# Optimization experiments

Hardware: AMD Instinct MI355X
Metric: run time of the kernel (lower is better)

## Reference

```python
import jax, jax.numpy as jnp
import numpy as np

BN_EPS = 1e-5

def _conv1x1(x, w, b):
    # x: [B,C,H,W], w: [O,C], b: [O]
    return jnp.einsum('bchw,oc->bohw', x, w) + b[None, :, None, None]

def _maxpool2x2(x):
    B, C, H, W = x.shape
    return x.reshape(B, C, H // 2, 2, W // 2, 2).max(axis=(3, 5))

def setup_inputs() -> dict:
    key = jax.random.key(0)
    ks = jax.random.split(key, 6)
    B, C, H, W = 8, 256, 64, 64
    Ci = C // 2  # inter_channels default
    x = jax.random.normal(ks[0], (B, C, H, W), jnp.float32)
    s = lambda k, sh: jax.random.normal(k, sh, jnp.float32) * 0.02
    return {
        'x': x,
        'w_g': s(ks[1], (Ci, C)), 'b_g': jnp.zeros((Ci,), jnp.float32),
        'w_theta': s(ks[2], (Ci, C)), 'b_theta': jnp.zeros((Ci,), jnp.float32),
        'w_phi': s(ks[3], (Ci, C)), 'b_phi': jnp.zeros((Ci,), jnp.float32),
        'w_w': s(ks[4], (C, Ci)), 'b_w': jnp.zeros((C,), jnp.float32),
        'bn_gamma': 1.0 + 0.1 * jax.random.normal(ks[5], (C,), jnp.float32),
        'bn_beta': jnp.zeros((C,), jnp.float32),
    }

def reference(x, w_g, b_g, w_theta, b_theta, w_phi, b_phi, w_w, b_w, bn_gamma, bn_beta):
    B, C, H, W = x.shape
    Ci = w_g.shape[0]
    # projections (sub_sample=True: maxpool 2x2 on g and phi)
    g_x = _maxpool2x2(_conv1x1(x, w_g, b_g)).reshape(B, Ci, -1)          # [B,Ci,M]
    g_x = g_x.transpose(0, 2, 1)                                          # [B,M,Ci]
    theta_x = _conv1x1(x, w_theta, b_theta).reshape(B, Ci, -1)            # [B,Ci,N]
    theta_x = theta_x.transpose(0, 2, 1)                                  # [B,N,Ci]
    phi_x = _maxpool2x2(_conv1x1(x, w_phi, b_phi)).reshape(B, Ci, -1)     # [B,Ci,M]
    # unscaled embedded-Gaussian attention (no 1/sqrt(d), as in source)
    f = jnp.einsum('bnc,bcm->bnm', theta_x, phi_x)                        # [B,N,M]
    f_div_C = jax.nn.softmax(f, axis=-1)
    y = jnp.einsum('bnm,bmc->bnc', f_div_C, g_x)                          # [B,N,Ci]
    y = y.transpose(0, 2, 1).reshape(B, Ci, H, W)
    # W: 1x1 conv + BatchNorm (training mode: batch statistics)
    wy = _conv1x1(y, w_w, b_w)                                            # [B,C,H,W]
    mean = wy.mean(axis=(0, 2, 3), keepdims=True)
    var = wy.var(axis=(0, 2, 3), keepdims=True)
    wy = (wy - mean) * jax.lax.rsqrt(var + BN_EPS)
    wy = wy * bn_gamma[None, :, None, None] + bn_beta[None, :, None, None]
    return wy + x
```

## Files before the change

### kernel.cpp

```cpp
#include <hip/hip_runtime.h>
#include <hip/hip_bf16.h>

#define NB 8
#define NC 256
#define NCI 128
#define NSP 4096
#define NM 1024

typedef float f32x4 __attribute__((ext_vector_type(4)));
typedef float f32x16 __attribute__((ext_vector_type(16)));
typedef short s16x8 __attribute__((ext_vector_type(8)));
typedef unsigned short u16;

#define OFF_XH  (0ull)
#define OFF_THT (33554432ull)
#define OFF_PHT (41943040ull)
#define OFF_GP  (44040192ull)
#define OFF_YH  (46137344ull)
#define OFF_YL  (54525952ull)
#define OFF_WY  (0ull)
#define OFF_WBH (62914560ull)
#define OFF_WBL (63111168ull)
#define OFF_WWH (63307776ull)
#define OFF_WWL (63373312ull)
#define OFF_S   (63438848ull)

#define GLL(src, dst) __builtin_amdgcn_global_load_lds( \
    (const __attribute__((address_space(1))) unsigned*)(src), \
    (__attribute__((address_space(3))) unsigned*)(dst), 16, 0, 0)

__device__ __forceinline__ u16 f2bf(float f) {
  union { __hip_bfloat16 h; u16 u; } v;
  v.h = __float2bfloat16(f);
  return v.u;
}
__device__ __forceinline__ float bf2f(u16 u) {
  union { unsigned u; float f; } v;
  v.u = (unsigned)u << 16;
  return v.f;
}
__device__ __forceinline__ u16 bfmax4(u16 a, u16 b, u16 c, u16 d) {
  float v = fmaxf(fmaxf(bf2f(a), bf2f(b)), fmaxf(bf2f(c), bf2f(d)));
  return f2bf(v);
}
__device__ __forceinline__ unsigned cvtpk(float lo, float hi) {
  unsigned r;
  asm volatile("v_cvt_pk_bf16_f32 %0, %1, %2" : "=v"(r) : "v"(lo), "v"(hi));
  return r;
}

__global__ void zero_stats(float* s) { s[threadIdx.x] = 0.f; }

__global__ __launch_bounds__(256) void wcvt(
    const float* __restrict__ wg, const float* __restrict__ wth,
    const float* __restrict__ wph, const float* __restrict__ ww,
    u16* __restrict__ wbh, u16* __restrict__ wbl,
    u16* __restrict__ wwh, u16* __restrict__ wwl)
{
  int idx = blockIdx.x * 256 + threadIdx.x;
  if (idx < 384 * 256) {
    int row = idx >> 8, k = idx & 255;
    float v = row < 128 ? wg[row * 256 + k]
            : row < 256 ? wth[(row - 128) * 256 + k]
                        : wph[(row - 256) * 256 + k];
    u16 h = f2bf(v);
    wbh[idx] = h;
    wbl[idx] = f2bf(v - bf2f(h));
  } else {
    int j = idx - 384 * 256;
    float v = ww[j];
    u16 h = f2bf(v);
    wwh[j] = h;
    wwl[j] = f2bf(v - bf2f(h));
  }
}

__global__ __launch_bounds__(256) void xt_cvt(const float* __restrict__ x,
                                              u16* __restrict__ xh)
{
  __shared__ float t[64 * 68];
  const int n0 = blockIdx.x << 6, c0 = blockIdx.y << 6, b = blockIdx.z;
  const int tid = threadIdx.x;
  const int cl = tid >> 4, n4 = (tid & 15) << 2;
#pragma unroll
  for (int it = 0; it < 4; ++it) {
    int c = it * 16 + cl;
    float4 v = *(const float4*)&x[((size_t)(b * NC + c0 + c)) * NSP + n0 + n4];
    *(float4*)&t[c * 68 + n4] = v;
  }
  __syncthreads();
#pragma unroll
  for (int it = 0; it < 2; ++it) {
    int task = it * 256 + tid;
    int n = task >> 3, cc = (task & 7) << 3;
    u16 oh[8];
#pragma unroll
    for (int i = 0; i < 8; ++i) oh[i] = f2bf(t[(cc + i) * 68 + n]);
    *(s16x8*)&xh[((size_t)(b * NSP + n0 + n)) * NC + c0 + cc] = *(s16x8*)oh;
  }
}

__global__ __launch_bounds__(512, 1) void proj_fused(
    const u16* __restrict__ xh,
    const u16* __restrict__ wbh, const u16* __restrict__ wbl,
    const float* __restrict__ bg, const float* __restrict__ bth,
    const float* __restrict__ bph,
    u16* __restrict__ thT, u16* __restrict__ phT, u16* __restrict__ gp)
{
  __shared__ char smem[116224];
  u16* xsh = (u16*)smem;
  u16* wsh = (u16*)(smem + 16384);
  u16* wsl = (u16*)(smem + 65536);
  u16* outl = (u16*)smem;
  float* bias = (float*)(smem + 114688);

  const int b = blockIdx.y, h2 = blockIdx.x;
  const int n0 = h2 << 7;
  const int tid = threadIdx.x;
  const int wave = tid >> 6, lane = tid & 63;
  const int lo16 = lane & 15, hi4 = lane >> 4;
  const int wr = wave >> 1, wc = wave & 1;
  const int obase = wr * 96, nbase = wc * 64;

  if (tid < 384)
    bias[tid] = tid < 128 ? bg[tid] : tid < 256 ? bth[tid - 128] : bph[tid - 256];

  f32x4 acc[6][4];
#pragma unroll
  for (int i = 0; i < 6; ++i)
#pragma unroll
    for (int j = 0; j < 4; ++j) acc[i][j] = (f32x4){0.f, 0.f, 0.f, 0.f};

  for (int step = 0; step < 4; ++step) {
    __syncthreads();
#pragma unroll
    for (int i = 0; i < 2; ++i) {
      int ci = i * 512 + tid;
      int n = ci >> 3, slot = ci & 7;
      size_t rowb = ((size_t)(b * NSP + n0 + n)) * 512 + step * 128 + ((slot ^ (n & 7)) << 4);
      GLL((const char*)xh + rowb, (char*)xsh + (size_t)(i * 512 + (tid & ~63)) * 16);
    }
#pragma unroll
    for (int i = 0; i < 6; ++i) {
      int ci = i * 512 + tid;
      int o = ci >> 3, slot = ci & 7;
      size_t rowb = (size_t)o * 512 + step * 128 + ((slot ^ (o & 7)) << 4);
      GLL((const char*)wbh + rowb, (char*)wsh + (size_t)(i * 512 + (tid & ~63)) * 16);
      GLL((const char*)wbl + rowb, (char*)wsl + (size_t)(i * 512 + (tid & ~63)) * 16);
    }
    __syncthreads();

#pragma unroll
    for (int kc = 0; kc < 2; ++kc) {
      const int sl = kc * 4 + hi4;
      s16x8 bfh[4];
#pragma unroll
      for (int fn = 0; fn < 4; ++fn) {
        int n = nbase + fn * 16 + lo16;
        bfh[fn] = *(const s16x8*)((const char*)xsh + (int)n * 128 + ((sl ^ (n & 7)) << 4));
      }
      __builtin_amdgcn_s_setprio(1);
#pragma unroll
      for (int fo = 0; fo < 6; ++fo) {
        int o = obase + fo * 16 + lo16;
        int off = (int)o * 128 + ((sl ^ (o & 7)) << 4);
        s16x8 afh = *(const s16x8*)((const char*)wsh + off);
        s16x8 afl = *(const s16x8*)((const char*)wsl + off);
#pragma unroll
        for (int fn = 0; fn < 4; ++fn) {
          acc[fo][fn] = __builtin_amdgcn_mfma_f32_16x16x32_bf16(afh, bfh[fn], acc[fo][fn], 0, 0, 0);
          acc[fo][fn] = __builtin_amdgcn_mfma_f32_16x16x32_bf16(afl, bfh[fn], acc[fo][fn], 0, 0, 0);
        }
      }
      __builtin_amdgcn_s_setprio(0);
    }
  }

  __syncthreads();
#pragma unroll
  for (int fo = 0; fo < 6; ++fo) {
    int orow = obase + fo * 16 + hi4 * 4;
    f32x4 bv = *(const f32x4*)&bias[orow];
#pragma unroll
    for (int fn = 0; fn < 4; ++fn) {
      int n = nbase + fn * 16 + lo16;
#pragma unroll
      for (int r = 0; r < 4; ++r)
        outl[(orow + r) * 137 + n] = f2bf(acc[fo][fn][r] + bv[r]);
    }
  }
  __syncthreads();

#pragma unroll
  for (int it = 0; it < 4; ++it) {
    int task = it * 512 + tid;
    int n = task >> 4, cc = (task & 15) << 3;
    u16 o[8];
#pragma unroll
    for (int i = 0; i < 8; ++i) o[i] = outl[(128 + cc + i) * 137 + n];
    *(s16x8*)&thT[((size_t)(b * NSP + n0 + n)) * NCI + cc] = *(s16x8*)o;
  }
  {
    int c = tid >> 2, wq = tid & 3;
    u16 o[8];
#pragma unroll
    for (int j = 0; j < 8; ++j) {
      int w2 = wq * 8 + j;
      o[j] = bfmax4(outl[c * 137 + 2 * w2], outl[c * 137 + 2 * w2 + 1],
                    outl[c * 137 + 64 + 2 * w2], outl[c * 137 + 64 + 2 * w2 + 1]);
    }
    *(s16x8*)&gp[((size_t)(b * NCI + c)) * NM + (h2 << 5) + wq * 8] = *(s16x8*)o;
  }
  {
    int w2 = tid >> 4, cc = (tid & 15) << 3;
    u16 o[8];
#pragma unroll
    for (int i = 0; i < 8; ++i) {
      int c = 256 + cc + i;
      o[i] = bfmax4(outl[c * 137 + 2 * w2], outl[c * 137 + 2 * w2 + 1],
                    outl[c * 137 + 64 + 2 * w2], outl[c * 137 + 64 + 2 * w2 + 1]);
    }
    *(s16x8*)&phT[((size_t)(b * NM + (h2 << 5) + w2)) * NCI + cc] = *(s16x8*)o;
  }
}

__global__ __launch_bounds__(512, 4) void attn_mfma(
    const u16* __restrict__ thT, const u16* __restrict__ phT,
    const u16* __restrict__ gP, u16* __restrict__ yh, u16* __restrict__ yl)
{
  __shared__ char smem[65536];

  const int b = blockIdx.y;
  const int n0 = blockIdx.x << 6;
  const int tid = threadIdx.x;
  const int wave = tid >> 6;
  const int qg = wave & 1;
  const int ch = (wave >> 1) & 1;
  const int kh = wave >> 2;
  const int lane = tid & 63;
  const int l31 = lane & 31;
  const int hi1 = lane >> 5;
  const int qbase = n0 + (qg << 5);
  const int swl = (l31 & 7) << 4;
  const int gsw = ((l31 >> 1) & 3) << 4;

  s16x8 thb[8];
  {
    const u16* tr = &thT[((size_t)b * NSP + qbase + l31) * NCI + hi1 * 8];
#pragma unroll
    for (int kc = 0; kc < 8; ++kc) thb[kc] = *(const s16x8*)&tr[kc * 16];
  }

  f32x16 yacc[2];
#pragma unroll
  for (int j = 0; j < 2; ++j) yacc[j] = (f32x16)0.f;
  float m_i = -3e38f, l_i = 0.f;

  auto stage = [&](int s, int step) {
    char* base = smem + s * 32768;
#pragma unroll
    for (int it = 0; it < 4; ++it) {
      const int kr = it >> 1;
      const int part = it & 1;
      const int m0 = kr * 512 + step * 32;
      char* dst = base + kr * 16384 + part * 8192 + (size_t)(tid & ~63) * 16;
      if (part == 0) {
        int m = tid >> 4, cb = (tid & 15) << 4;
        const char* src = (const char*)phT + (((size_t)b * NM + m0 + m) << 8) + (cb ^ ((m & 7) << 4));
        GLL(src, dst);
      } else {
        int c = tid >> 2, mb = (tid & 3) << 4;
        const char* src = (const char*)gP + (((size_t)b * NCI + c) << 11) + m0 * 2 + (mb ^ (((c >> 1) & 3) << 4));
        GLL(src, dst);
      }
    }
  };

  stage(0, 0);
  __syncthreads();
  int cur = 0;

  for (int step = 0; step < 16; ++step) {
    if (step < 15) stage(cur ^ 1, step + 1);
    const char* ph = smem + cur * 32768 + kh * 16384;
    const char* gg = ph + 8192;

    f32x16 s0 = (f32x16)0.f;
    __builtin_amdgcn_s_setprio(1);
#pragma unroll
    for (int kc = 0; kc < 8; ++kc) {
      s16x8 a0 = *(const s16x8*)(ph + l31 * 256 + ((kc * 32 + hi1 * 16) ^ swl));
      s0 = __builtin_amdgcn_mfma_f32_32x32x16_bf16(a0, thb[kc], s0, 0, 0, 0);
    }
    __builtin_amdgcn_s_setprio(0);

    float pm = s0[0];
#pragma unroll
    for (int i = 1; i < 16; ++i) pm = fmaxf(pm, s0[i]);
    pm = fmaxf(pm, __shfl_xor(pm, 32));
    float mn = fmaxf(m_i, pm);
    float sc = __expf(m_i - mn);
    float rs = 0.f;
#pragma unroll
    for (int i = 0; i < 16; ++i) { s0[i] = __expf(s0[i] - mn); rs += s0[i]; }
    rs += __shfl_xor(rs, 32);
    l_i = l_i * sc + rs;
    m_i = mn;
#pragma unroll
    for (int j = 0; j < 2; ++j)
#pragma unroll
      for (int i = 0; i < 16; ++i) yacc[j][i] *= sc;

    s16x8 pb[2];
#pragma unroll
    for (int km = 0; km < 2; ++km) {
      int r0 = km * 8;
      unsigned X0 = cvtpk(s0[r0 + 0], s0[r0 + 1]);
      unsigned X1 = cvtpk(s0[r0 + 2], s0[r0 + 3]);
      unsigned X2 = cvtpk(s0[r0 + 4], s0[r0 + 5]);
      unsigned X3 = cvtpk(s0[r0 + 6], s0[r0 + 7]);
      asm volatile("v_permlane32_swap_b32 %0, %1" : "+v"(X0), "+v"(X2));
      asm volatile("v_permlane32_swap_b32 %0, %1" : "+v"(X1), "+v"(X3));
      unsigned d[4] = {X0, X1, X2, X3};
      pb[km] = *(s16x8*)d;
    }

    __builtin_amdgcn_s_setprio(1);
#pragma unroll
    for (int j = 0; j < 2; ++j) {
      const char* grow = gg + (ch * 64 + j * 32 + l31) * 64;
#pragma unroll
      for (int km = 0; km < 2; ++km) {
        s16x8 ga = *(const s16x8*)(grow + ((km * 32 + hi1 * 16) ^ gsw));
        yacc[j] = __builtin_amdgcn_mfma_f32_32x32x16_bf16(ga, pb[km], yacc[j], 0, 0, 0);
      }
    }
    __builtin_amdgcn_s_setprio(0);

    __syncthreads();
    cur ^= 1;
  }

  const int w2 = wave & 3;
  float* yx = (float*)(smem + w2 * 8192);
  float* ml = (float*)(smem + 32768 + w2 * 512);
  if (kh == 1) {
#pragma unroll
    for (int j = 0; j < 2; ++j)
#pragma unroll
      for (int i4 = 0; i4 < 4; ++i4) {
        f32x4 v = {yacc[j][i4 * 4 + 0], yacc[j][i4 * 4 + 1],
                   yacc[j][i4 * 4 + 2], yacc[j][i4 * 4 + 3]};
        *(f32x4*)((char*)yx + (size_t)((j * 4 + i4) * 64 + lane) * 16) = v;
      }
    ml[lane * 2] = m_i;
    ml[lane * 2 + 1] = l_i;
  }
  __syncthreads();
  if (kh == 1) return;

  {
    float m1 = ml[lane * 2], l1 = ml[lane * 2 + 1];
    float mm = fmaxf(m_i, m1);
    float sc0 = __expf(m_i - mm), sc1 = __expf(m1 - mm);
    float inv = 1.f / (l_i * sc0 + l1 * sc1);
    float a0 = sc0 * inv, a1 = sc1 * inv;
#pragma unroll
    for (int j = 0; j < 2; ++j)
#pragma unroll
      for (int i4 = 0; i4 < 4; ++i4) {
        f32x4 v = *(const f32x4*)((const char*)yx + (size_t)((j * 4 + i4) * 64 + lane) * 16);
#pragma unroll
        for (int k = 0; k < 4; ++k)
          yacc[j][i4 * 4 + k] = yacc[j][i4 * 4 + k] * a0 + v[k] * a1;
      }
  }

  u16* bounce = (u16*)(smem + 36864) + w2 * 2304;
  const int qq0 = lane >> 3, cb8 = (lane & 7) << 3;
#pragma unroll
  for (int pass = 0; pass < 2; ++pass) {
#pragma unroll
    for (int j = 0; j < 2; ++j) {
#pragma unroll
      for (int rp = 0; rp < 8; ++rp) {
        int r = rp * 2;
        int cl = j * 32 + (r & 3) + 8 * (r >> 2) + 4 * hi1;
        float v0 = yacc[j][r], v1 = yacc[j][r + 1];
        u16 h0 = f2bf(v0), h1 = f2bf(v1);
        u16 w0 = h0, w1 = h1;
        if (pass) { w0 = f2bf(v0 - bf2f(h0)); w1 = f2bf(v1 - bf2f(h1)); }
        *(unsigned*)&bounce[l31 * 72 + cl] = (unsigned)w0 | ((unsigned)w1 << 16);
      }
    }
    asm volatile("s_waitcnt lgkmcnt(0)" ::: "memory");
    u16* dst = pass ? yl : yh;
    size_t base = ((size_t)b * NSP + qbase) * NCI + ch * 64 + cb8;
#pragma unroll
    for (int it = 0; it < 4; ++it) {
      int row = qq0 + it * 8;
      *(s16x8*)&dst[base + (size_t)row * NCI] = *(const s16x8*)&bounce[row * 72 + cb8];
    }
    asm volatile("s_waitcnt lgkmcnt(0)" ::: "memory");
  }
}

__global__ __launch_bounds__(512, 1) void conv_w_mfma(
    const u16* __restrict__ yh, const u16* __restrict__ yl,
    const u16* __restrict__ wwh, const u16* __restrict__ wwl,
    const float* __restrict__ bw, float* __restrict__ wy,
    float* __restrict__ s1g, float* __restrict__ s2g)
{
  __shared__ char smem[102400];
  u16* wsh = (u16*)smem;
  u16* wsl = (u16*)(smem + 32768);
  u16* ysh = (u16*)(smem + 65536);
  u16* ysl = (u16*)(smem + 81920);
  float (*sums1)[256] = (float(*)[256])(smem + 98304);
  float (*sums2)[256] = (float(*)[256])(smem + 100352);

  const int b = blockIdx.y, n0 = blockIdx.x << 7;
  const int tid = threadIdx.x;
  const int wave = tid >> 6, lane = tid & 63;
  const int lo16 = lane & 15, hi4 = lane >> 4;
  const int wr = wave >> 1, wc = wave & 1;
  const int obase = wr * 64, nbase = wc * 64;

  f32x4 acc[4][4];
#pragma unroll
  for (int i = 0; i < 4; ++i)
#pragma unroll
    for (int j = 0; j < 4; ++j) acc[i][j] = (f32x4){0.f, 0.f, 0.f, 0.f};

  for (int step = 0; step < 2; ++step) {
    __syncthreads();
#pragma unroll
    for (int i = 0; i < 4; ++i) {
      int ci = i * 512 + tid;
      int o = ci >> 3, slot = ci & 7;
      size_t rowb = (size_t)o * 256 + step * 128 + ((slot ^ (o & 7)) << 4);
      GLL((const char*)wwh + rowb, (char*)wsh + (size_t)(i * 512 + (tid & ~63)) * 16);
      GLL((const char*)wwl + rowb, (char*)wsl + (size_t)(i * 512 + (tid & ~63)) * 16);
    }
#pragma unroll
    for (int i = 0; i < 2; ++i) {
      int ci = i * 512 + tid;
      int n = ci >> 3, slot = ci & 7;
      size_t rowb = ((size_t)(b * NSP + n0 + n)) * 256 + step * 128 + ((slot ^ (n & 7)) << 4);
      GLL((const char*)yh + rowb, (char*)ysh + (size_t)(i * 512 + (tid & ~63)) * 16);
      GLL((const char*)yl + rowb, (char*)ysl + (size_t)(i * 512 + (tid & ~63)) * 16);
    }
    __syncthreads();

#pragma unroll
    for (int kc = 0; kc < 2; ++kc) {
      const int sl = kc * 4 + hi4;
      s16x8 bfh[4], bfl[4];
#pragma unroll
      for (int fn = 0; fn < 4; ++fn) {
        int n = nbase + fn * 16 + lo16;
        int off = (int)n * 128 + ((sl ^ (n & 7)) << 4);
        bfh[fn] = *(const s16x8*)((const char*)ysh + off);
        bfl[fn] = *(const s16x8*)((const char*)ysl + off);
      }
      __builtin_amdgcn_s_setprio(1);
#pragma unroll
      for (int fo = 0; fo < 4; ++fo) {
        int o = obase + fo * 16 + lo16;
        int off = (int)o * 128 + ((sl ^ (o & 7)) << 4);
        s16x8 afh = *(const s16x8*)((const char*)wsh + off);
        s16x8 afl = *(const s16x8*)((const char*)wsl + off);
#pragma unroll
        for (int fn = 0; fn < 4; ++fn) {
          acc[fo][fn] = __builtin_amdgcn_mfma_f32_16x16x32_bf16(afh, bfh[fn], acc[fo][fn], 0, 0, 0);
          acc[fo][fn] = __builtin_amdgcn_mfma_f32_16x16x32_bf16(afh, bfl[fn], acc[fo][fn], 0, 0, 0);
          acc[fo][fn] = __builtin_amdgcn_mfma_f32_16x16x32_bf16(afl, bfh[fn], acc[fo][fn], 0, 0, 0);
        }
      }
      __builtin_amdgcn_s_setprio(0);
    }
  }

#pragma unroll
  for (int fo = 0; fo < 4; ++fo) {
    int orow = obase + fo * 16 + hi4 * 4;
    float bv[4];
#pragma unroll
    for (int r = 0; r < 4; ++r) bv[r] = bw[orow + r];
    float ss[4] = {0.f, 0.f, 0.f, 0.f}, sq[4] = {0.f, 0.f, 0.f, 0.f};
#pragma unroll
    for (int fn = 0; fn < 4; ++fn) {
      int col = n0 + nbase + fn * 16 + lo16;
#pragma unroll
      for (int r = 0; r < 4; ++r) {
        float v = acc[fo][fn][r] + bv[r];
        wy[((size_t)(b * NC) + orow + r) * NSP + col] = v;
        ss[r] += v;
        sq[r] += v * v;
      }
    }
#pragma unroll
    for (int r = 0; r < 4; ++r) {
#pragma unroll
      for (int d = 1; d < 16; d <<= 1) {
        ss[r] += __shfl_xor(ss[r], d);
        sq[r] += __shfl_xor(sq[r], d);
      }
    }
    if (lo16 == 0) {
#pragma unroll
      for (int r = 0; r < 4; ++r) {
        sums1[wc][orow + r] = ss[r];
        sums2[wc][orow + r] = sq[r];
      }
    }
  }
  __syncthreads();
  if (tid < 256) {
    atomicAdd(&s1g[tid], sums1[0][tid] + sums1[1][tid]);
    atomicAdd(&s2g[tid], sums2[0][tid] + sums2[1][tid]);
  }
}

__global__ __launch_bounds__(256) void bn_res4(
    const float* __restrict__ wy, const float* __restrict__ x,
    const float* __restrict__ s1, const float* __restrict__ s2,
    const float* __restrict__ gamma, const float* __restrict__ beta,
    float* __restrict__ out)
{
  int i4 = (blockIdx.x * 256 + threadIdx.x) << 2;
  int c = (i4 >> 12) & 255;
  const float cnt = 1.f / 32768.f;
  float mean = s1[c] * cnt;
  float var = s2[c] * cnt - mean * mean;
  float inv = rsqrtf(var + 1e-5f) * gamma[c];
  float bet = beta[c];
  float4 w = *(const float4*)&wy[i4];
  float4 xv = *(const float4*)&x[i4];
  float4 o;
  o.x = (w.x - mean) * inv + bet + xv.x;
  o.y = (w.y - mean) * inv + bet + xv.y;
  o.z = (w.z - mean) * inv + bet + xv.z;
  o.w = (w.w - mean) * inv + bet + xv.w;
  *(float4*)&out[i4] = o;
}

extern "C" void kernel_launch(void* const* d_in, const int* in_sizes, int n_in,
                              void* d_out, int out_size, void* d_ws, size_t ws_size,
                              hipStream_t stream) {
  const float* x    = (const float*)d_in[0];
  const float* w_g  = (const float*)d_in[1];
  const float* b_g  = (const float*)d_in[2];
  const float* w_th = (const float*)d_in[3];
  const float* b_th = (const float*)d_in[4];
  const float* w_ph = (const float*)d_in[5];
  const float* b_ph = (const float*)d_in[6];
  const float* w_w  = (const float*)d_in[7];
  const float* b_w  = (const float*)d_in[8];
  const float* gam  = (const float*)d_in[9];
  const float* bet  = (const float*)d_in[10];
  float* out = (float*)d_out;
  char* ws = (char*)d_ws;

  u16*   xh  = (u16*)(ws + OFF_XH);
  u16*   thT = (u16*)(ws + OFF_THT);
  u16*   phT = (u16*)(ws + OFF_PHT);
  u16*   gp  = (u16*)(ws + OFF_GP);
  u16*   yhb = (u16*)(ws + OFF_YH);
  u16*   ylb = (u16*)(ws + OFF_YL);
  float* wy  = (float*)(ws + OFF_WY);
  u16*   wbh = (u16*)(ws + OFF_WBH);
  u16*   wbl = (u16*)(ws + OFF_WBL);
  u16*   wwh = (u16*)(ws + OFF_WWH);
  u16*   wwl = (u16*)(ws + OFF_WWL);
  float* s1  = (float*)(ws + OFF_S);
  float* s2  = s1 + 256;

  wcvt<<<dim3(512), 256, 0, stream>>>(w_g, w_th, w_ph, w_w, wbh, wbl, wwh, wwl);
  zero_stats<<<dim3(1), 512, 0, stream>>>(s1);
  xt_cvt<<<dim3(64, 4, 8), 256, 0, stream>>>(x, xh);

  proj_fused<<<dim3(32, 8), 512, 0, stream>>>(xh, wbh, wbl, b_g, b_th, b_ph, thT, phT, gp);

  attn_mfma<<<dim3(64, 8), 512, 0, stream>>>(thT, phT, gp, yhb, ylb);

  conv_w_mfma<<<dim3(32, 8), 512, 0, stream>>>(yhb, ylb, wwh, wwl, b_w, wy, s1, s2);

  bn_res4<<<dim3(8192), 256, 0, stream>>>(wy, x, s1, s2, gam, bet, out);
}
```

Before: 113.0 us.

## Halve attention block waves, each covering all channels; add lazy softmax rescale

Measured after the change: 106.9 us. 1.06x faster.

```diff
diff --git a/kernel.cpp b/kernel.cpp
--- a/kernel.cpp
+++ b/kernel.cpp
@@ -224,7 +224,7 @@
   }
 }
 
-__global__ __launch_bounds__(512, 4) void attn_mfma(
+__global__ __launch_bounds__(256, 2) void attn_mfma(
     const u16* __restrict__ thT, const u16* __restrict__ phT,
     const u16* __restrict__ gP, u16* __restrict__ yh, u16* __restrict__ yl)
 {
@@ -235,8 +235,7 @@
   const int tid = threadIdx.x;
   const int wave = tid >> 6;
   const int qg = wave & 1;
-  const int ch = (wave >> 1) & 1;
-  const int kh = wave >> 2;
+  const int kh = wave >> 1;
   const int lane = tid & 63;
   const int l31 = lane & 31;
   const int hi1 = lane >> 5;
@@ -251,25 +250,28 @@
     for (int kc = 0; kc < 8; ++kc) thb[kc] = *(const s16x8*)&tr[kc * 16];
   }
 
-  f32x16 yacc[2];
-#pragma unroll
-  for (int j = 0; j < 2; ++j) yacc[j] = (f32x16)0.f;
+  f32x16 yacc[4];
+#pragma unroll
+  for (int ct = 0; ct < 4; ++ct) yacc[ct] = (f32x16)0.f;
   float m_i = -3e38f, l_i = 0.f;
 
   auto stage = [&](int s, int step) {
     char* base = smem + s * 32768;
 #pragma unroll
-    for (int it = 0; it < 4; ++it) {
-      const int kr = it >> 1;
-      const int part = it & 1;
+    for (int it = 0; it < 8; ++it) {
+      const int kr = it >> 2;
+      const int part = (it >> 1) & 1;
+      const int half = it & 1;
       const int m0 = kr * 512 + step * 32;
-      char* dst = base + kr * 16384 + part * 8192 + (size_t)(tid & ~63) * 16;
+      int ci = half * 256 + tid;
+      char* dst = base + kr * 16384 + part * 8192 +
+                  (size_t)(half * 256 + (tid & ~63)) * 16;
       if (part == 0) {
-        int m = tid >> 4, cb = (tid & 15) << 4;
+        int m = ci >> 4, cb = (ci & 15) << 4;
         const char* src = (const char*)phT + (((size_t)b * NM + m0 + m) << 8) + (cb ^ ((m & 7) << 4));
         GLL(src, dst);
       } else {
-        int c = tid >> 2, mb = (tid & 3) << 4;
+        int c = ci >> 2, mb = (ci & 3) << 4;
         const char* src = (const char*)gP + (((size_t)b * NCI + c) << 11) + m0 * 2 + (mb ^ (((c >> 1) & 3) << 4));
         GLL(src, dst);
       }
@@ -298,18 +300,21 @@
 #pragma unroll
     for (int i = 1; i < 16; ++i) pm = fmaxf(pm, s0[i]);
     pm = fmaxf(pm, __shfl_xor(pm, 32));
-    float mn = fmaxf(m_i, pm);
-    float sc = __expf(m_i - mn);
+    if (!__all(pm - m_i <= 8.0f)) {
+      float mn = fmaxf(m_i, pm);
+      float sc = __expf(m_i - mn);
+      l_i *= sc;
+      m_i = mn;
+#pragma unroll
+      for (int ct = 0; ct < 4; ++ct)
+#pragma unroll
+        for (int i = 0; i < 16; ++i) yacc[ct][i] *= sc;
+    }
     float rs = 0.f;
 #pragma unroll
-    for (int i = 0; i < 16; ++i) { s0[i] = __expf(s0[i] - mn); rs += s0[i]; }
+    for (int i = 0; i < 16; ++i) { s0[i] = __expf(s0[i] - m_i); rs += s0[i]; }
     rs += __shfl_xor(rs, 32);
-    l_i = l_i * sc + rs;
-    m_i = mn;
-#pragma unroll
-    for (int j = 0; j < 2; ++j)
-#pragma unroll
-      for (int i = 0; i < 16; ++i) yacc[j][i] *= sc;
+    l_i += rs;
 
     s16x8 pb[2];
 #pragma unroll
@@ -327,12 +332,12 @@
 
     __builtin_amdgcn_s_setprio(1);
 #pragma unroll
-    for (int j = 0; j < 2; ++j) {
-      const char* grow = gg + (ch * 64 + j * 32 + l31) * 64;
+    for (int ct = 0; ct < 4; ++ct) {
+      const char* grow = gg + (ct * 32 + l31) * 64;
 #pragma unroll
       for (int km = 0; km < 2; ++km) {
         s16x8 ga = *(const s16x8*)(grow + ((km * 32 + hi1 * 16) ^ gsw));
-        yacc[j] = __builtin_amdgcn_mfma_f32_32x32x16_bf16(ga, pb[km], yacc[j], 0, 0, 0);
+        yacc[ct] = __builtin_amdgcn_mfma_f32_32x32x16_bf16(ga, pb[km], yacc[ct], 0, 0, 0);
       }
     }
     __builtin_amdgcn_s_setprio(0);
@@ -341,17 +346,16 @@
     cur ^= 1;
   }
 
-  const int w2 = wave & 3;
-  float* yx = (float*)(smem + w2 * 8192);
-  float* ml = (float*)(smem + 32768 + w2 * 512);
+  float* yx = (float*)(smem + qg * 16384);
+  float* ml = (float*)(smem + 32768 + qg * 512);
   if (kh == 1) {
 #pragma unroll
-    for (int j = 0; j < 2; ++j)
+    for (int ct = 0; ct < 4; ++ct)
 #pragma unroll
       for (int i4 = 0; i4 < 4; ++i4) {
-        f32x4 v = {yacc[j][i4 * 4 + 0], yacc[j][i4 * 4 + 1],
-                   yacc[j][i4 * 4 + 2], yacc[j][i4 * 4 + 3]};
-        *(f32x4*)((char*)yx + (size_t)((j * 4 + i4) * 64 + lane) * 16) = v;
+        f32x4 v = {yacc[ct][i4 * 4 + 0], yacc[ct][i4 * 4 + 1],
+                   yacc[ct][i4 * 4 + 2], yacc[ct][i4 * 4 + 3]};
+        *(f32x4*)((char*)yx + (size_t)((ct * 4 + i4) * 64 + lane) * 16) = v;
       }
     ml[lane * 2] = m_i;
     ml[lane * 2 + 1] = l_i;
@@ -366,41 +370,39 @@
     float inv = 1.f / (l_i * sc0 + l1 * sc1);
     float a0 = sc0 * inv, a1 = sc1 * inv;
 #pragma unroll
-    for (int j = 0; j < 2; ++j)
+    for (int ct = 0; ct < 4; ++ct)
 #pragma unroll
       for (int i4 = 0; i4 < 4; ++i4) {
-        f32x4 v = *(const f32x4*)((const char*)yx + (size_t)((j * 4 + i4) * 64 + lane) * 16);
-#pragma unroll
-        for (int k = 0; k < 4; ++k)
-          yacc[j][i4 * 4 + k] = yacc[j][i4 * 4 + k] * a0 + v[k] * a1;
-      }
-  }
-
-  u16* bounce = (u16*)(smem + 36864) + w2 * 2304;
-  const int qq0 = lane >> 3, cb8 = (lane & 7) << 3;
+        f32x4 v = *(const f32x4*)((const char*)yx + (size_t)((ct * 4 + i4) * 64 + lane) * 16);
+#pragma unroll
+        for (int j = 0; j < 4; ++j)
+          yacc[ct][i4 * 4 + j] = yacc[ct][i4 * 4 + j] * a0 + v[j] * a1;
+      }
+  }
+
+  u16* bounce = (u16*)(smem + 34816) + qg * 4224;
+  const int qq = lane >> 1, c0 = (lane & 1) << 6;
 #pragma unroll
   for (int pass = 0; pass < 2; ++pass) {
 #pragma unroll
-    for (int j = 0; j < 2; ++j) {
+    for (int ct = 0; ct < 4; ++ct) {
 #pragma unroll
       for (int rp = 0; rp < 8; ++rp) {
         int r = rp * 2;
-        int cl = j * 32 + (r & 3) + 8 * (r >> 2) + 4 * hi1;
-        float v0 = yacc[j][r], v1 = yacc[j][r + 1];
+        int c = ct * 32 + (r & 3) + 8 * (r >> 2) + 4 * hi1;
+        float v0 = yacc[ct][r], v1 = yacc[ct][r + 1];
         u16 h0 = f2bf(v0), h1 = f2bf(v1);
         u16 w0 = h0, w1 = h1;
         if (pass) { w0 = f2bf(v0 - bf2f(h0)); w1 = f2bf(v1 - bf2f(h1)); }
-        *(unsigned*)&bounce[l31 * 72 + cl] = (unsigned)w0 | ((unsigned)w1 << 16);
+        *(unsigned*)&bounce[l31 * 132 + c] = (unsigned)w0 | ((unsigned)w1 << 16);
       }
     }
     asm volatile("s_waitcnt lgkmcnt(0)" ::: "memory");
     u16* dst = pass ? yl : yh;
-    size_t base = ((size_t)b * NSP + qbase) * NCI + ch * 64 + cb8;
-#pragma unroll
-    for (int it = 0; it < 4; ++it) {
-      int row = qq0 + it * 8;
-      *(s16x8*)&dst[base + (size_t)row * NCI] = *(const s16x8*)&bounce[row * 72 + cb8];
-    }
+    size_t row = ((size_t)b * NSP + qbase + qq) * NCI + c0;
+#pragma unroll
+    for (int k = 0; k < 8; ++k)
+      *(s16x8*)&dst[row + k * 8] = *(const s16x8*)&bounce[qq * 132 + c0 + k * 8];
     asm volatile("s_waitcnt lgkmcnt(0)" ::: "memory");
   }
 }
@@ -582,7 +584,7 @@
 
   proj_fused<<<dim3(32, 8), 512, 0, stream>>>(xh, wbh, wbl, b_g, b_th, b_ph, thT, phT, gp);
 
-  attn_mfma<<<dim3(64, 8), 512, 0, stream>>>(thT, phT, gp, yhb, ylb);
+  attn_mfma<<<dim3(64, 8), 256, 0, stream>>>(thT, phT, gp, yhb, ylb);
 
   conv_w_mfma<<<dim3(32, 8), 512, 0, stream>>>(yhb, ylb, wwh, wwl, b_w, wy, s1, s2);
 
```
